# Kernel tuning notes

Hardware: AMD Instinct MI355X
Metric: run time of the kernel (lower is better)

## Reference

```python
import jax, jax.numpy as jnp
import numpy as np

CMD, LIDAR, H, T = 2, 360, 256, 50
B = 2048


def _cell(x, h, c, Wih, Whh, b):
    # PyTorch LSTM: gates ordered (i, f, g, o)
    g = x @ Wih.T + h @ Whh.T + b
    i, f, gg, o = jnp.split(g, 4, axis=-1)
    c = jax.nn.sigmoid(f) * c + jax.nn.sigmoid(i) * jnp.tanh(gg)
    h = jax.nn.sigmoid(o) * jnp.tanh(c)
    return h, c


def setup_inputs() -> dict:
    key = jax.random.key(0)
    ks = jax.random.split(key, 10)
    s = 0.05  # small init so tanh/sigmoid stay in sane range
    return {
        "past_data": jax.random.normal(ks[0], (B, T, CMD + LIDAR), jnp.float32),
        "future_cmds": jax.random.normal(ks[1], (B, T, CMD), jnp.float32),
        "enc_Wih": jax.random.normal(ks[2], (4 * H, CMD + LIDAR), jnp.float32) * s,
        "enc_Whh": jax.random.normal(ks[3], (4 * H, H), jnp.float32) * s,
        "enc_b": jax.random.normal(ks[4], (4 * H,), jnp.float32) * s,
        "dec_Wih": jax.random.normal(ks[5], (4 * H, LIDAR + CMD), jnp.float32) * s,
        "dec_Whh": jax.random.normal(ks[6], (4 * H, H), jnp.float32) * s,
        "dec_b": jax.random.normal(ks[7], (4 * H,), jnp.float32) * s,
        "out_W": jax.random.normal(ks[8], (LIDAR, H), jnp.float32) * s,
        "out_b": jax.random.normal(ks[9], (LIDAR,), jnp.float32) * s,
    }


def reference(past_data, future_cmds, enc_Wih, enc_Whh, enc_b,
              dec_Wih, dec_Whh, dec_b, out_W, out_b):
    b = past_data.shape[0]
    h0 = jnp.zeros((b, H), past_data.dtype)
    c0 = jnp.zeros((b, H), past_data.dtype)

    # ---- encoder LSTM over past_data ----
    def enc_step(carry, x):
        h, c = carry
        h, c = _cell(x, h, c, enc_Wih, enc_Whh, enc_b)
        return (h, c), None

    (h, c), _ = jax.lax.scan(enc_step, (h0, c0), jnp.swapaxes(past_data, 0, 1))

    lidar0 = past_data[:, -1, CMD:]  # [B, LIDAR]

    def dec_step(carry, cmd):
        h, c, lidar = carry
        x = jnp.concatenate([lidar, cmd], axis=-1)  # [B, LIDAR+CMD]
        h, c = _cell(x, h, c, dec_Wih, dec_Whh, dec_b)
        lidar = h @ out_W.T + out_b
        return (h, c, lidar), lidar

    _, preds = jax.lax.scan(dec_step, (h, c, lidar0), jnp.swapaxes(future_cmds, 0, 1))
    return jnp.swapaxes(preds, 0, 1)  # [B, T, LIDAR]
```

## Files before the change

### kernel.cpp

```cpp
#include <hip/hip_runtime.h>
#include <hip/hip_bf16.h>
#include <math.h>

#define CMDN   2
#define LIDARN 360
#define HN     256
#define TN     50
#define BATCH  2048
#define KXN    362
#define NG     1024
#define KP     384
#define MR     (TN*BATCH)
#define SLAB   ((size_t)BATCH*HN)
#define NOF    24

typedef __attribute__((ext_vector_type(8))) short bf16x8;
typedef __attribute__((ext_vector_type(4))) float f32x4;

__device__ inline unsigned short f2b(float f) {
    unsigned int x = __builtin_bit_cast(unsigned int, f);
    x += 0x7FFFu + ((x >> 16) & 1u);
    return (unsigned short)(x >> 16);
}
__device__ inline float b2f(unsigned short u) {
    unsigned int x = ((unsigned int)u) << 16;
    return __builtin_bit_cast(float, x);
}
__device__ inline float sigf(float x)  { return 1.f / (1.f + __expf(-x)); }
__device__ inline float tanhfa(float x){ return 2.f / (1.f + __expf(-2.f * x)) - 1.f; }

__device__ inline int p2j(int p) { return ((p & 3) << 8) + (p >> 2); }

typedef const __attribute__((address_space(1))) unsigned int* gp1_t;
typedef __attribute__((address_space(3))) unsigned int* lp3_t;
__device__ inline void gload16(const void* g, void* l) {
    __builtin_amdgcn_global_load_lds((gp1_t)g, (lp3_t)l, 16, 0, 0);
}

__global__ __launch_bounds__(256) void pack_xb(
    const float* __restrict__ past, unsigned short* __restrict__ Xb)
{
    int c = blockIdx.x * 256 + threadIdx.x;
    if (c >= MR * (KP / 8)) return;
    int r = c / (KP / 8), kc = c - r * (KP / 8);
    int b = r & 2047, t = r >> 11;
    const float* p = past + ((size_t)b * TN + t) * KXN;
    const int k = kc * 8;
    bf16x8 v;
    if (k + 8 <= KXN) {
        float2 f0 = *(const float2*)(p + k);
        float2 f1 = *(const float2*)(p + k + 2);
        float2 f2 = *(const float2*)(p + k + 4);
        float2 f3 = *(const float2*)(p + k + 6);
        v[0] = (short)f2b(f0.x); v[1] = (short)f2b(f0.y);
        v[2] = (short)f2b(f1.x); v[3] = (short)f2b(f1.y);
        v[4] = (short)f2b(f2.x); v[5] = (short)f2b(f2.y);
        v[6] = (short)f2b(f3.x); v[7] = (short)f2b(f3.y);
    } else {
        #pragma unroll
        for (int e = 0; e < 8; ++e)
            v[e] = (k + e < KXN) ? (short)f2b(p[k + e]) : (short)0;
    }
    *(bf16x8*)&Xb[(size_t)r * KP + k] = v;
}

template<int OMODE>
__global__ __launch_bounds__(256) void gemm_fast(
    const unsigned short* __restrict__ A,
    const unsigned short* __restrict__ B,
    const float* __restrict__ bias,
    void* __restrict__ Cv, int K, int ldc)
{
    __shared__ __align__(16) unsigned short As[128 * 32];
    __shared__ __align__(16) unsigned short Bs[128 * 32];

    const int nwg = gridDim.x * gridDim.y;
    const int hid = blockIdx.y * gridDim.x + blockIdx.x;
    const int lid = (hid & 7) * (nwg >> 3) + (hid >> 3);
    const int bx  = lid % gridDim.x;
    const int by  = lid / gridDim.x;

    const int tid  = threadIdx.x;
    const int lane = tid & 63;
    const int wv   = tid >> 6;
    const int wm   = wv >> 1, wn = wv & 1;
    const int r0   = by * 128;
    const int n0   = bx * 128;
    const int l15  = lane & 15;
    const int lhi  = lane >> 4;

    const int srow = lane >> 2;
    const int sc   = lane & 3;

    f32x4 acc[4][4] = {};

    for (int k0 = 0; k0 < K; k0 += 32) {
        #pragma unroll
        for (int j = 0; j < 2; ++j) {
            const int rl = (wv * 2 + j) * 16 + srow;
            const int cs = sc ^ (rl & 3);
            gload16(&A[(size_t)(r0 + rl) * K + k0 + cs * 8], &As[(wv * 2 + j) * 512]);
            gload16(&B[(size_t)(n0 + rl) * K + k0 + cs * 8], &Bs[(wv * 2 + j) * 512]);
        }
        __syncthreads();
        bf16x8 a[4], b[4];
        #pragma unroll
        for (int i = 0; i < 4; ++i) {
            const int ra = wm * 64 + i * 16 + l15;
            const int rb = wn * 64 + i * 16 + l15;
            a[i] = *(const bf16x8*)&As[ra * 32 + (lhi ^ (ra & 3)) * 8];
            b[i] = *(const bf16x8*)&Bs[rb * 32 + (lhi ^ (rb & 3)) * 8];
        }
        #pragma unroll
        for (int mi = 0; mi < 4; ++mi)
            #pragma unroll
            for (int ni = 0; ni < 4; ++ni)
                acc[mi][ni] = __builtin_amdgcn_mfma_f32_16x16x32_bf16(a[mi], b[ni], acc[mi][ni], 0, 0, 0);
        __syncthreads();
    }

    #pragma unroll
    for (int mi = 0; mi < 4; ++mi) {
        const int rowb = r0 + wm * 64 + mi * 16 + ((lane >> 4) << 2);
        #pragma unroll
        for (int ni = 0; ni < 4; ++ni) {
            const int col = n0 + wn * 64 + ni * 16 + l15;
            #pragma unroll
            for (int r = 0; r < 4; ++r) {
                const int row = rowb + r;
                float v = acc[mi][ni][r];
                if (OMODE == 0) {
                    ((float*)Cv)[(size_t)row * ldc + col] = v + bias[col];
                } else if (OMODE == 2) {
                    ((unsigned short*)Cv)[(size_t)row * ldc + col] = f2b(v + bias[col]);
                } else {
                    if (col < LIDARN)
                        ((float*)Cv)[(size_t)row * (TN * LIDARN) + (size_t)(TN - 1) * LIDARN + col]
                            = v + bias[col];
                }
            }
        }
    }
}

template<int MODE>
__global__ __launch_bounds__(512) void step3(
    const unsigned short* __restrict__ hsrc,
    const unsigned short* __restrict__ Wf,
    const unsigned short* __restrict__ addb,
    const float* __restrict__ biasf,
    const float* __restrict__ cmdw,
    const float* __restrict__ cmds_t,
    const unsigned short* __restrict__ oWf,
    const float* __restrict__ ob,
    float* __restrict__ out,
    int tprev,
    float* __restrict__ cst,
    unsigned short* __restrict__ hdst)
{
    __shared__ __align__(16) unsigned short Hl[64 * 264];
    __shared__ __align__(16) unsigned short Xl[64 * 128];
    __shared__ float cmdl[64][2];

    const int tid  = threadIdx.x;
    const int lane = tid & 63;
    const int w    = tid >> 6;
    const int l15  = lane & 15;
    const int lhi  = lane >> 4;
    const int g    = l15 & 3;
    const int cg   = blockIdx.x >> 5;
    const int rg   = blockIdx.x & 31;
    const int r0   = rg * 64;

    #pragma unroll
    for (int i = 0; i < 4; ++i) {
        const int c = i * 512 + tid;
        const int row = c >> 5, col8 = c & 31;
        *(bf16x8*)&Hl[row * 264 + col8 * 8] =
            *(const bf16x8*)&hsrc[(size_t)(r0 + row) * HN + col8 * 8];
    }
    if (MODE <= 1) {
        const unsigned short* xs = addb + (size_t)r0 * NG + cg * 128;
        #pragma unroll
        for (int i = 0; i < 2; ++i) {
            const int c = i * 512 + tid;
            const int row = c >> 4, col8 = c & 15;
            *(bf16x8*)&Xl[row * 128 + col8 * 8] =
                *(const bf16x8*)&xs[(size_t)row * NG + col8 * 8];
        }
    }
    if (MODE >= 1 && tid < 64) {
        const float2 cv = *(const float2*)&cmds_t[(size_t)(r0 + tid) * (TN * CMDN)];
        cmdl[tid][0] = cv.x; cmdl[tid][1] = cv.y;
    }
    __syncthreads();

    const unsigned short* wb = Wf + (size_t)(cg * 8 + w) * 4096;
    f32x4 acc[4] = {};
    #pragma unroll
    for (int kf = 0; kf < 8; ++kf) {
        bf16x8 b = *(const bf16x8*)&wb[(size_t)(kf * 64 + lane) * 8];
        #pragma unroll
        for (int mf = 0; mf < 4; ++mf) {
            bf16x8 a = *(const bf16x8*)&Hl[(mf * 16 + l15) * 264 + kf * 32 + lhi * 8];
            acc[mf] = __builtin_amdgcn_mfma_f32_16x16x32_bf16(a, b, acc[mf], 0, 0, 0);
        }
    }

    f32x4 acc_o0 = {}, acc_o1 = {};
    const int mf_o = w >> 1;
    const int nf0  = (w & 1) ? 2 : 0;
    const int nfn  = (w & 1) ? 1 : 2;
    if (MODE == 2) {
        #pragma unroll
        for (int kf = 0; kf < 8; ++kf) {
            bf16x8 a = *(const bf16x8*)&Hl[(mf_o * 16 + l15) * 264 + kf * 32 + lhi * 8];
            const int f0 = cg * 3 + nf0;
            bf16x8 b0 = *(const bf16x8*)&oWf[(size_t)((f0 * 8 + kf) * 64 + lane) * 8];
            acc_o0 = __builtin_amdgcn_mfma_f32_16x16x32_bf16(a, b0, acc_o0, 0, 0, 0);
            if (nfn == 2) {
                bf16x8 b1 = *(const bf16x8*)&oWf[(size_t)(((f0 + 1) * 8 + kf) * 64 + lane) * 8];
                acc_o1 = __builtin_amdgcn_mfma_f32_16x16x32_bf16(a, b1, acc_o1, 0, 0, 0);
            }
        }
    }

    const int p = cg * 128 + w * 16 + l15;
    const int u = cg * 32 + w * 4 + (l15 >> 2);
    float w0_r = 0.f, w1_r = 0.f, bf_r = 0.f;
    if (MODE >= 1) { w0_r = cmdw[p * 2]; w1_r = cmdw[p * 2 + 1]; }
    if (MODE == 2) bf_r = biasf[p];
    #pragma unroll
    for (int mf = 0; mf < 4; ++mf)
        #pragma unroll
        for (int r = 0; r < 4; ++r) {
            const int rw = mf * 16 + lhi * 4 + r;
            float v = acc[mf][r];
            if (MODE <= 1) v += b2f(Xl[rw * 128 + w * 16 + l15]);
            if (MODE == 2) v += bf_r;
            if (MODE >= 1) v += cmdl[rw][0] * w0_r + cmdl[rw][1] * w1_r;
            float act = (g == 2) ? tanhfa(v) : sigf(v);
            float a1 = __shfl_xor(act, 1);
            float a2 = __shfl_xor(act, 2);
            float a3 = __shfl_xor(act, 3);
            if (g == 0) {
                const size_t idx = (size_t)(r0 + rw) * HN + u;
                float cc = a1 * cst[idx] + act * a2;
                cst[idx] = cc;
                hdst[idx] = f2b(a3 * tanhfa(cc));
            }
        }

    if (MODE == 2) {
        #pragma unroll
        for (int i = 0; i < 2; ++i) {
            if (i < nfn) {
                const int col = (cg * 3 + nf0 + i) * 16 + l15;
                if (col < LIDARN) {
                    const float bo = ob[col];
                    const f32x4 ao = i ? acc_o1 : acc_o0;
                    #pragma unroll
                    for (int r = 0; r < 4; ++r) {
                        const int brow = r0 + mf_o * 16 + lhi * 4 + r;
                        out[(size_t)brow * (TN * LIDARN) + (size_t)tprev * LIDARN + col]
                            = ao[r] + bo;
                    }
                }
            }
        }
    }
}

__global__ __launch_bounds__(256) void pack_w(
    const float* __restrict__ past,
    const float* __restrict__ eWih, const float* __restrict__ eb,
    const float* __restrict__ dWih, const float* __restrict__ db,
    const float* __restrict__ oW,
    unsigned short* __restrict__ L0b,
    unsigned short* __restrict__ Wihe_p,
    unsigned short* __restrict__ Wdihl_p,
    unsigned short* __restrict__ oWp,
    float* __restrict__ Wc_p,
    float* __restrict__ ebp, float* __restrict__ dbp)
{
    int idx = blockIdx.x * 256 + threadIdx.x;
    if (idx < BATCH * KP) {
        int b = idx / KP, k = idx - b * KP;
        L0b[idx] = (k < LIDARN)
            ? f2b(past[((size_t)b * TN + (TN - 1)) * KXN + CMDN + k]) : (unsigned short)0;
    }
    if (idx < NG * KP) {
        int p = idx / KP, k = idx - p * KP;
        int j = p2j(p);
        Wihe_p[idx]  = (k < KXN)    ? f2b(eWih[(size_t)j * KXN + k]) : (unsigned short)0;
        Wdihl_p[idx] = (k < LIDARN) ? f2b(dWih[(size_t)j * KXN + k]) : (unsigned short)0;
        if (k < 2) Wc_p[p * 2 + k] = dWih[(size_t)j * KXN + LIDARN + k];
        if (k == 0) { ebp[p] = eb[j]; dbp[p] = db[j]; }
    }
    if (idx < KP * HN) {
        int n = idx / HN, k = idx - n * HN;
        oWp[idx] = (n < LIDARN) ? f2b(oW[(size_t)n * HN + k]) : (unsigned short)0;
    }
}

__global__ __launch_bounds__(256) void wcomb_kernel(
    const float* __restrict__ dWih, const float* __restrict__ dWhh,
    const float* __restrict__ oW, float* __restrict__ Wcomb_f)
{
    const int pb = blockIdx.x * 4, k = threadIdx.x;
    int j0 = p2j(pb), j1 = p2j(pb + 1), j2 = p2j(pb + 2), j3 = p2j(pb + 3);
    float s0 = dWhh[(size_t)j0 * HN + k];
    float s1 = dWhh[(size_t)j1 * HN + k];
    float s2 = dWhh[(size_t)j2 * HN + k];
    float s3 = dWhh[(size_t)j3 * HN + k];
    #pragma unroll 4
    for (int n = 0; n < LIDARN; ++n) {
        const float ow = oW[(size_t)n * HN + k];
        s0 += dWih[(size_t)j0 * KXN + n] * ow;
        s1 += dWih[(size_t)j1 * KXN + n] * ow;
        s2 += dWih[(size_t)j2 * KXN + n] * ow;
        s3 += dWih[(size_t)j3 * KXN + n] * ow;
    }
    Wcomb_f[(size_t)pb * HN + k]            = s0;
    Wcomb_f[(size_t)(pb + 1) * HN + k]      = s1;
    Wcomb_f[(size_t)(pb + 2) * HN + k]      = s2;
    Wcomb_f[(size_t)(pb + 3) * HN + k]      = s3;
}

__global__ __launch_bounds__(256) void biasf_kernel(
    const float* __restrict__ dWih, const float* __restrict__ db,
    const float* __restrict__ ob, float* __restrict__ biasf)
{
    int p = blockIdx.x * 256 + threadIdx.x;
    if (p >= NG) return;
    int j = p2j(p);
    float s = db[j];
    for (int n = 0; n < LIDARN; ++n)
        s += dWih[(size_t)j * KXN + n] * ob[n];
    biasf[p] = s;
}

__global__ __launch_bounds__(256) void pack_wfrag(
    const float* __restrict__ eWhh, const float* __restrict__ dWhh,
    const float* __restrict__ Wcomb_f,
    unsigned short* __restrict__ Wf_enc,
    unsigned short* __restrict__ Wf_dec0,
    unsigned short* __restrict__ Wf_dec)
{
    const int NW = NG * HN;
    int idx = blockIdx.x * 256 + threadIdx.x;
    if (idx >= 3 * NW) return;
    int sel = idx / NW;
    int d   = idx - sel * NW;
    int e    = d & 7;
    int lane = (d >> 3) & 63;
    int kf   = (d >> 9) & 7;
    int cf   = d >> 12;
    int p = cf * 16 + (lane & 15);
    int k = kf * 32 + (lane >> 4) * 8 + e;
    if (sel == 0)      Wf_enc[d]  = f2b(eWhh[(size_t)p2j(p) * HN + k]);
    else if (sel == 1) Wf_dec0[d] = f2b(dWhh[(size_t)p2j(p) * HN + k]);
    else               Wf_dec[d]  = f2b(Wcomb_f[(size_t)p * HN + k]);
}

__global__ __launch_bounds__(256) void pack_owf(
    const float* __restrict__ oW, unsigned short* __restrict__ oWf)
{
    int d = blockIdx.x * 256 + threadIdx.x;
    if (d >= NOF * 8 * 64 * 8) return;
    int e = d & 7, lane = (d >> 3) & 63, kf = (d >> 9) & 7, f = d >> 12;
    int n = f * 16 + (lane & 15);
    int k = kf * 32 + (lane >> 4) * 8 + e;
    oWf[d] = (n < LIDARN) ? f2b(oW[(size_t)n * HN + k]) : (unsigned short)0;
}

__global__ __launch_bounds__(256) void init_hc(
    unsigned short* __restrict__ h0, float* __restrict__ cst)
{
    int idx = blockIdx.x * 256 + threadIdx.x;
    if (idx < BATCH * HN) { h0[idx] = 0; cst[idx] = 0.f; }
}

extern "C" void kernel_launch(void* const* d_in, const int* in_sizes, int n_in,
                              void* d_out, int out_size, void* d_ws, size_t ws_size,
                              hipStream_t stream)
{
    const float* past = (const float*)d_in[0];
    const float* cmds = (const float*)d_in[1];
    const float* eWih = (const float*)d_in[2];
    const float* eWhh = (const float*)d_in[3];
    const float* eb   = (const float*)d_in[4];
    const float* dWih = (const float*)d_in[5];
    const float* dWhh = (const float*)d_in[6];
    const float* db   = (const float*)d_in[7];
    const float* oW   = (const float*)d_in[8];
    const float* ob   = (const float*)d_in[9];
    float* out = (float*)d_out;

    char* w = (char*)d_ws;
    auto alloc = [&](size_t bytes) {
        char* p = w; w += (bytes + 255) & ~(size_t)255; return p;
    };
    unsigned short* xw      = (unsigned short*)alloc((size_t)MR * NG * 2);
    unsigned short* Xb      = (unsigned short*)alloc((size_t)MR * KP * 2);
    unsigned short* hdec    = (unsigned short*)alloc((size_t)MR * HN * 2);
    unsigned short* l0wb    = (unsigned short*)alloc((size_t)BATCH * NG * 2);
    unsigned short* hpp     = (unsigned short*)alloc(2 * SLAB * 2);
    float*          cst     = (float*)alloc(SLAB * 4);
    float*          Wcomb_f = (float*)alloc((size_t)NG * HN * 4);
    unsigned short* Wf_enc  = (unsigned short*)alloc((size_t)NG * HN * 2);
    unsigned short* Wf_dec0 = (unsigned short*)alloc((size_t)NG * HN * 2);
    unsigned short* Wf_dec  = (unsigned short*)alloc((size_t)NG * HN * 2);
    unsigned short* oWf     = (unsigned short*)alloc((size_t)NOF * 8 * 64 * 8 * 2);
    unsigned short* L0b     = (unsigned short*)alloc((size_t)BATCH * KP * 2);
    unsigned short* Wihe_p  = (unsigned short*)alloc((size_t)NG * KP * 2);
    unsigned short* Wdihl_p = (unsigned short*)alloc((size_t)NG * KP * 2);
    unsigned short* oWp     = (unsigned short*)alloc((size_t)KP * HN * 2);
    float*          Wc_p    = (float*)alloc((size_t)NG * 2 * 4);
    float*          ebp     = (float*)alloc(NG * 4);
    float*          dbp     = (float*)alloc(NG * 4);
    float*          biasf   = (float*)alloc(NG * 4);

    pack_w<<<(BATCH * KP + 255) / 256, 256, 0, stream>>>(
        past, eWih, eb, dWih, db, oW,
        L0b, Wihe_p, Wdihl_p, oWp, Wc_p, ebp, dbp);
    wcomb_kernel<<<NG / 4, 256, 0, stream>>>(dWih, dWhh, oW, Wcomb_f);
    biasf_kernel<<<(NG + 255) / 256, 256, 0, stream>>>(dWih, db, ob, biasf);
    pack_wfrag<<<(3 * NG * HN + 255) / 256, 256, 0, stream>>>(
        eWhh, dWhh, Wcomb_f, Wf_enc, Wf_dec0, Wf_dec);
    pack_owf<<<(NOF * 8 * 64 * 8 + 255) / 256, 256, 0, stream>>>(oW, oWf);
    init_hc<<<(BATCH * HN + 255) / 256, 256, 0, stream>>>(hpp, cst);
    pack_xb<<<(MR * (KP / 8) + 255) / 256, 256, 0, stream>>>(past, Xb);

    gemm_fast<2><<<dim3(NG / 128, MR / 128), 256, 0, stream>>>(
        Xb, Wihe_p, ebp, xw, KP, NG);
    gemm_fast<2><<<dim3(NG / 128, BATCH / 128), 256, 0, stream>>>(
        L0b, Wdihl_p, dbp, l0wb, KP, NG);

    for (int t = 0; t < TN; ++t) {
        const unsigned short* hs = hpp + (size_t)(t & 1) * SLAB;
        unsigned short*       hd = hpp + (size_t)((t + 1) & 1) * SLAB;
        step3<0><<<256, 512, 0, stream>>>(
            hs, Wf_enc, xw + (size_t)t * BATCH * NG,
            nullptr, nullptr, nullptr, nullptr, nullptr, nullptr, 0, cst, hd);
    }
    step3<1><<<256, 512, 0, stream>>>(
        hpp + (size_t)(TN & 1) * SLAB, Wf_dec0, l0wb,
        nullptr, Wc_p, cmds, nullptr, nullptr, nullptr, 0, cst, hdec);
    for (int t = 1; t < TN; ++t) {
        step3<2><<<256, 512, 0, stream>>>(
            hdec + (size_t)(t - 1) * SLAB, Wf_dec, nullptr,
            biasf, Wc_p, cmds + (size_t)t * CMDN,
            oWf, ob, out, t - 1, cst, hdec + (size_t)t * SLAB);
    }
    gemm_fast<3><<<dim3(KP / 128, BATCH / 128), 256, 0, stream>>>(
        hdec + (size_t)(TN - 1) * SLAB, oWp, ob, out, HN, 0);
}
```

Baseline: 1.368 ms.

## Halve per-block batch rows in LSTM step kernel and transpose cell-state layout

The recurrent step kernel now processes 32 batch rows per block instead of 64, doubling the grid from 256 to 512 blocks and adding a min-blocks launch bound so more blocks can be resident across the CUs. The cell state buffer is switched to a unit-major [H][B] layout so each lane reads and writes four consecutive rows as one vector instead of scattered scalars. The output projection is remapped so each wave handles one 16x16 tile. Smaller tiles reload the recurrent weight fragments twice as often per step, which adds L2 traffic in exchange for better CU coverage.

```diff
diff --git a/kernel.cpp b/kernel.cpp
--- a/kernel.cpp
+++ b/kernel.cpp
@@ -144,7 +144,7 @@
 }
 
 template<int MODE>
-__global__ __launch_bounds__(512) void step3(
+__global__ __launch_bounds__(512, 4) void step4(
     const unsigned short* __restrict__ hsrc,
     const unsigned short* __restrict__ Wf,
     const unsigned short* __restrict__ addb,
@@ -155,12 +155,12 @@
     const float* __restrict__ ob,
     float* __restrict__ out,
     int tprev,
-    float* __restrict__ cst,
+    float* __restrict__ ct,
     unsigned short* __restrict__ hdst)
 {
-    __shared__ __align__(16) unsigned short Hl[64 * 264];
-    __shared__ __align__(16) unsigned short Xl[64 * 128];
-    __shared__ float cmdl[64][2];
+    __shared__ __align__(16) unsigned short Hl[32 * 264];
+    __shared__ __align__(16) unsigned short Xl[32 * 128];
+    __shared__ float cmdl[32][2];
 
     const int tid  = threadIdx.x;
     const int lane = tid & 63;
@@ -168,12 +168,12 @@
     const int l15  = lane & 15;
     const int lhi  = lane >> 4;
     const int g    = l15 & 3;
-    const int cg   = blockIdx.x >> 5;
-    const int rg   = blockIdx.x & 31;
-    const int r0   = rg * 64;
+    const int cg   = blockIdx.x >> 6;
+    const int rg   = blockIdx.x & 63;
+    const int r0   = rg * 32;
 
     #pragma unroll
-    for (int i = 0; i < 4; ++i) {
+    for (int i = 0; i < 2; ++i) {
         const int c = i * 512 + tid;
         const int row = c >> 5, col8 = c & 31;
         *(bf16x8*)&Hl[row * 264 + col8 * 8] =
@@ -181,47 +181,38 @@
     }
     if (MODE <= 1) {
         const unsigned short* xs = addb + (size_t)r0 * NG + cg * 128;
-        #pragma unroll
-        for (int i = 0; i < 2; ++i) {
-            const int c = i * 512 + tid;
-            const int row = c >> 4, col8 = c & 15;
-            *(bf16x8*)&Xl[row * 128 + col8 * 8] =
-                *(const bf16x8*)&xs[(size_t)row * NG + col8 * 8];
-        }
-    }
-    if (MODE >= 1 && tid < 64) {
+        const int row = tid >> 4, col8 = tid & 15;
+        *(bf16x8*)&Xl[row * 128 + col8 * 8] =
+            *(const bf16x8*)&xs[(size_t)row * NG + col8 * 8];
+    }
+    if (MODE >= 1 && tid < 32) {
         const float2 cv = *(const float2*)&cmds_t[(size_t)(r0 + tid) * (TN * CMDN)];
         cmdl[tid][0] = cv.x; cmdl[tid][1] = cv.y;
     }
     __syncthreads();
 
     const unsigned short* wb = Wf + (size_t)(cg * 8 + w) * 4096;
-    f32x4 acc[4] = {};
+    f32x4 acc[2] = {};
     #pragma unroll
     for (int kf = 0; kf < 8; ++kf) {
         bf16x8 b = *(const bf16x8*)&wb[(size_t)(kf * 64 + lane) * 8];
         #pragma unroll
-        for (int mf = 0; mf < 4; ++mf) {
+        for (int mf = 0; mf < 2; ++mf) {
             bf16x8 a = *(const bf16x8*)&Hl[(mf * 16 + l15) * 264 + kf * 32 + lhi * 8];
             acc[mf] = __builtin_amdgcn_mfma_f32_16x16x32_bf16(a, b, acc[mf], 0, 0, 0);
         }
     }
 
-    f32x4 acc_o0 = {}, acc_o1 = {};
-    const int mf_o = w >> 1;
-    const int nf0  = (w & 1) ? 2 : 0;
-    const int nfn  = (w & 1) ? 1 : 2;
-    if (MODE == 2) {
+    f32x4 acc_o = {};
+    const int s_o = w & 1;
+    const int f_o = w >> 1;
+    if (MODE == 2 && f_o < 3) {
+        const int fg = cg * 3 + f_o;
         #pragma unroll
         for (int kf = 0; kf < 8; ++kf) {
-            bf16x8 a = *(const bf16x8*)&Hl[(mf_o * 16 + l15) * 264 + kf * 32 + lhi * 8];
-            const int f0 = cg * 3 + nf0;
-            bf16x8 b0 = *(const bf16x8*)&oWf[(size_t)((f0 * 8 + kf) * 64 + lane) * 8];
-            acc_o0 = __builtin_amdgcn_mfma_f32_16x16x32_bf16(a, b0, acc_o0, 0, 0, 0);
-            if (nfn == 2) {
-                bf16x8 b1 = *(const bf16x8*)&oWf[(size_t)(((f0 + 1) * 8 + kf) * 64 + lane) * 8];
-                acc_o1 = __builtin_amdgcn_mfma_f32_16x16x32_bf16(a, b1, acc_o1, 0, 0, 0);
-            }
+            bf16x8 a = *(const bf16x8*)&Hl[(s_o * 16 + l15) * 264 + kf * 32 + lhi * 8];
+            bf16x8 b = *(const bf16x8*)&oWf[(size_t)((fg * 8 + kf) * 64 + lane) * 8];
+            acc_o = __builtin_amdgcn_mfma_f32_16x16x32_bf16(a, b, acc_o, 0, 0, 0);
         }
     }
 
@@ -231,7 +222,9 @@
     if (MODE >= 1) { w0_r = cmdw[p * 2]; w1_r = cmdw[p * 2 + 1]; }
     if (MODE == 2) bf_r = biasf[p];
     #pragma unroll
-    for (int mf = 0; mf < 4; ++mf)
+    for (int mf = 0; mf < 2; ++mf) {
+        float* cp = (g == 0) ? &ct[(size_t)u * BATCH + r0 + mf * 16 + lhi * 4] : nullptr;
+        f32x4 c4 = (g == 0) ? *(const f32x4*)cp : f32x4{0.f, 0.f, 0.f, 0.f};
         #pragma unroll
         for (int r = 0; r < 4; ++r) {
             const int rw = mf * 16 + lhi * 4 + r;
@@ -244,28 +237,23 @@
             float a2 = __shfl_xor(act, 2);
             float a3 = __shfl_xor(act, 3);
             if (g == 0) {
-                const size_t idx = (size_t)(r0 + rw) * HN + u;
-                float cc = a1 * cst[idx] + act * a2;
-                cst[idx] = cc;
-                hdst[idx] = f2b(a3 * tanhfa(cc));
+                float cc = a1 * c4[r] + act * a2;
+                c4[r] = cc;
+                hdst[(size_t)(r0 + rw) * HN + u] = f2b(a3 * tanhfa(cc));
             }
         }
-
-    if (MODE == 2) {
-        #pragma unroll
-        for (int i = 0; i < 2; ++i) {
-            if (i < nfn) {
-                const int col = (cg * 3 + nf0 + i) * 16 + l15;
-                if (col < LIDARN) {
-                    const float bo = ob[col];
-                    const f32x4 ao = i ? acc_o1 : acc_o0;
-                    #pragma unroll
-                    for (int r = 0; r < 4; ++r) {
-                        const int brow = r0 + mf_o * 16 + lhi * 4 + r;
-                        out[(size_t)brow * (TN * LIDARN) + (size_t)tprev * LIDARN + col]
-                            = ao[r] + bo;
-                    }
-                }
+        if (g == 0) *(f32x4*)cp = c4;
+    }
+
+    if (MODE == 2 && f_o < 3) {
+        const int col = (cg * 3 + f_o) * 16 + l15;
+        if (col < LIDARN) {
+            const float bo = ob[col];
+            #pragma unroll
+            for (int r = 0; r < 4; ++r) {
+                const int brow = r0 + s_o * 16 + lhi * 4 + r;
+                out[(size_t)brow * (TN * LIDARN) + (size_t)tprev * LIDARN + col]
+                    = acc_o[r] + bo;
             }
         }
     }
@@ -375,10 +363,10 @@
 }
 
 __global__ __launch_bounds__(256) void init_hc(
-    unsigned short* __restrict__ h0, float* __restrict__ cst)
+    unsigned short* __restrict__ h0, float* __restrict__ ct)
 {
     int idx = blockIdx.x * 256 + threadIdx.x;
-    if (idx < BATCH * HN) { h0[idx] = 0; cst[idx] = 0.f; }
+    if (idx < BATCH * HN) { h0[idx] = 0; ct[idx] = 0.f; }
 }
 
 extern "C" void kernel_launch(void* const* d_in, const int* in_sizes, int n_in,
@@ -406,7 +394,7 @@
     unsigned short* hdec    = (unsigned short*)alloc((size_t)MR * HN * 2);
     unsigned short* l0wb    = (unsigned short*)alloc((size_t)BATCH * NG * 2);
     unsigned short* hpp     = (unsigned short*)alloc(2 * SLAB * 2);
-    float*          cst     = (float*)alloc(SLAB * 4);
+    float*          ct      = (float*)alloc(SLAB * 4);
     float*          Wcomb_f = (float*)alloc((size_t)NG * HN * 4);
     unsigned short* Wf_enc  = (unsigned short*)alloc((size_t)NG * HN * 2);
     unsigned short* Wf_dec0 = (unsigned short*)alloc((size_t)NG * HN * 2);
@@ -429,7 +417,7 @@
     pack_wfrag<<<(3 * NG * HN + 255) / 256, 256, 0, stream>>>(
         eWhh, dWhh, Wcomb_f, Wf_enc, Wf_dec0, Wf_dec);
     pack_owf<<<(NOF * 8 * 64 * 8 + 255) / 256, 256, 0, stream>>>(oW, oWf);
-    init_hc<<<(BATCH * HN + 255) / 256, 256, 0, stream>>>(hpp, cst);
+    init_hc<<<(BATCH * HN + 255) / 256, 256, 0, stream>>>(hpp, ct);
     pack_xb<<<(MR * (KP / 8) + 255) / 256, 256, 0, stream>>>(past, Xb);
 
     gemm_fast<2><<<dim3(NG / 128, MR / 128), 256, 0, stream>>>(
@@ -440,18 +428,18 @@
     for (int t = 0; t < TN; ++t) {
         const unsigned short* hs = hpp + (size_t)(t & 1) * SLAB;
         unsigned short*       hd = hpp + (size_t)((t + 1) & 1) * SLAB;
-        step3<0><<<256, 512, 0, stream>>>(
+        step4<0><<<512, 512, 0, stream>>>(
             hs, Wf_enc, xw + (size_t)t * BATCH * NG,
-            nullptr, nullptr, nullptr, nullptr, nullptr, nullptr, 0, cst, hd);
-    }
-    step3<1><<<256, 512, 0, stream>>>(
+            nullptr, nullptr, nullptr, nullptr, nullptr, nullptr, 0, ct, hd);
+    }
+    step4<1><<<512, 512, 0, stream>>>(
         hpp + (size_t)(TN & 1) * SLAB, Wf_dec0, l0wb,
-        nullptr, Wc_p, cmds, nullptr, nullptr, nullptr, 0, cst, hdec);
+        nullptr, Wc_p, cmds, nullptr, nullptr, nullptr, 0, ct, hdec);
     for (int t = 1; t < TN; ++t) {
-        step3<2><<<256, 512, 0, stream>>>(
+        step4<2><<<512, 512, 0, stream>>>(
             hdec + (size_t)(t - 1) * SLAB, Wf_dec, nullptr,
             biasf, Wc_p, cmds + (size_t)t * CMDN,
-            oWf, ob, out, t - 1, cst, hdec + (size_t)t * SLAB);
+            oWf, ob, out, t - 1, ct, hdec + (size_t)t * SLAB);
     }
     gemm_fast<3><<<dim3(KP / 128, BATCH / 128), 256, 0, stream>>>(
         hdec + (size_t)(TN - 1) * SLAB, oWp, ob, out, HN, 0);
```

After: 1.125 ms. 1.22x faster.
